# Kernel optimization log

Hardware: AMD Instinct MI355X
Metric: run time of the kernel (lower is better)

Reference implementation:

```python
import jax, jax.numpy as jnp
import numpy as np

N_NODES = 50000
N_EDGES = 600000
IN_CH = 64
HID = 128
N_GRAPHS = 64
EPS = 0.0  # GINEConv default eps


def setup_inputs() -> dict:
    key = jax.random.key(0)
    ks = jax.random.split(key, 16)
    x = jax.random.normal(ks[0], (N_NODES, IN_CH), dtype=jnp.float32)
    edge_index = jax.random.randint(ks[1], (2, N_EDGES), 0, N_NODES, dtype=jnp.int64)
    edge_attr = jax.random.normal(ks[2], (N_EDGES, 3), dtype=jnp.float32)
    batch = jnp.sort(jax.random.randint(ks[3], (N_NODES,), 0, N_GRAPHS, dtype=jnp.int64))
    s = lambda fan_in: 1.0 / np.sqrt(fan_in)
    # conv1: edge lin (3->IN_CH), mlp (IN_CH->HID->HID)
    el1_w = jax.random.uniform(ks[4], (3, IN_CH), minval=-s(3), maxval=s(3))
    el1_b = jnp.zeros((IN_CH,), jnp.float32)
    w1a = jax.random.uniform(ks[5], (IN_CH, HID), minval=-s(IN_CH), maxval=s(IN_CH))
    b1a = jnp.zeros((HID,), jnp.float32)
    w1b = jax.random.uniform(ks[6], (HID, HID), minval=-s(HID), maxval=s(HID))
    b1b = jnp.zeros((HID,), jnp.float32)
    # conv2: edge lin (3->HID), mlp (HID->HID->HID)
    el2_w = jax.random.uniform(ks[7], (3, HID), minval=-s(3), maxval=s(3))
    el2_b = jnp.zeros((HID,), jnp.float32)
    w2a = jax.random.uniform(ks[8], (HID, HID), minval=-s(HID), maxval=s(HID))
    b2a = jnp.zeros((HID,), jnp.float32)
    w2b = jax.random.uniform(ks[9], (HID, HID), minval=-s(HID), maxval=s(HID))
    b2b = jnp.zeros((HID,), jnp.float32)
    return dict(x=x, edge_index=edge_index, edge_attr=edge_attr, batch=batch,
                el1_w=el1_w, el1_b=el1_b, w1a=w1a, b1a=b1a, w1b=w1b, b1b=b1b,
                el2_w=el2_w, el2_b=el2_b, w2a=w2a, b2a=b2a, w2b=w2b, b2b=b2b)


def _gine_conv(x, src, dst, edge_attr, el_w, el_b, wa, ba, wb, bb):
    # message: relu(x_j + Lin(edge_attr)), aggregated (sum) at target nodes
    e = edge_attr @ el_w + el_b              # [E, d]
    msg = jax.nn.relu(x[src] + e)            # [E, d]
    agg = jax.ops.segment_sum(msg, dst, num_segments=x.shape[0])  # [N, d]
    h = (1.0 + EPS) * x + agg
    h = jax.nn.relu(h @ wa + ba) @ wb + bb   # MLP
    return h


def reference(x, edge_index, edge_attr, batch,
              el1_w, el1_b, w1a, b1a, w1b, b1b,
              el2_w, el2_b, w2a, b2a, w2b, b2b):
    src, dst = edge_index[0], edge_index[1]
    h = jax.nn.relu(_gine_conv(x, src, dst, edge_attr, el1_w, el1_b, w1a, b1a, w1b, b1b))
    h = jax.nn.relu(_gine_conv(h, src, dst, edge_attr, el2_w, el2_b, w2a, b2a, w2b, b2b))
    # global mean pool per graph
    sums = jax.ops.segment_sum(h, batch, num_segments=N_GRAPHS)
    cnt = jax.ops.segment_sum(jnp.ones((h.shape[0],), h.dtype), batch, num_segments=N_GRAPHS)
    return sums / jnp.maximum(cnt, 1.0)[:, None]
```

## Files before the change

kernel.cpp:

```cpp
#include <hip/hip_runtime.h>

#define N_NODES 50000
#define N_EDGES 600000
#define N_PAD 50048
#define IN_CH 64
#define HID 128
#define N_GRAPHS 64
#define CAP 64
#define CAP_SHIFT 6
#define BUILD_BLOCKS ((N_EDGES + 255) / 256)
#define PREP_BLOCKS  ((N_NODES * IN_CH / 4) / 256)

typedef __attribute__((ext_vector_type(8))) short bf16x8;
typedef __attribute__((ext_vector_type(4))) float f32x4;

__device__ __forceinline__ float bf2f(unsigned short u) {
    union { unsigned int i; float f; } v; v.i = ((unsigned int)u) << 16; return v.f;
}
__device__ __forceinline__ unsigned short f2bf(float f) {
    union { float f; unsigned int i; } v; v.f = f;
    unsigned int u = v.i;
    return (unsigned short)((u + 0x7FFFu + ((u >> 16) & 1u)) >> 16);
}


__global__ void prep_build_kernel(const float* __restrict__ x,
                                  const int* __restrict__ ei,
                                  const float* __restrict__ ea,
                                  const int* __restrict__ batch,
                                  const float* __restrict__ w1a, const float* __restrict__ w1b,
                                  const float* __restrict__ w2a, const float* __restrict__ w2b,
                                  unsigned short* __restrict__ xbf,
                                  unsigned short* __restrict__ waT1, unsigned short* __restrict__ wbT1,
                                  unsigned short* __restrict__ waT2, unsigned short* __restrict__ wbT2,
                                  int* __restrict__ deg, uint2* __restrict__ edata,
                                  float* __restrict__ out, float* __restrict__ inv_cnt) {
    const int b = blockIdx.x;
    if (b < BUILD_BLOCKS) {
        int i = b * 256 + threadIdx.x;
        if (i >= N_EDGES) return;
        int s = ei[i];
        int d = ei[N_EDGES + i];
        float a0 = ea[3 * (size_t)i], a1 = ea[3 * (size_t)i + 1], a2 = ea[3 * (size_t)i + 2];
        int p = atomicAdd(&deg[d], 1);
        if (p < CAP)
            edata[((size_t)d << CAP_SHIFT) + p] =
                make_uint2((unsigned)s | ((unsigned)f2bf(a0) << 16),
                           (unsigned)f2bf(a1) | ((unsigned)f2bf(a2) << 16));
    } else {
        int i = (b - BUILD_BLOCKS) * 256 + threadIdx.x;
        if (i < N_NODES * IN_CH / 4) {
            float4 v = ((const float4*)x)[i];
            uint2 o;
            o.x = (unsigned)f2bf(v.x) | ((unsigned)f2bf(v.y) << 16);
            o.y = (unsigned)f2bf(v.z) | ((unsigned)f2bf(v.w) << 16);
            ((uint2*)xbf)[i] = o;
        }
        if (i < N_GRAPHS * HID) out[i] = 0.f;
        if (i < N_GRAPHS) {
            int g = i;
            int lo = 0, hi = N_NODES;
            while (lo < hi) { int mid = (lo + hi) >> 1; if (batch[mid] < g) lo = mid + 1; else hi = mid; }
            int start = lo;
            lo = 0; hi = N_NODES;
            while (lo < hi) { int mid = (lo + hi) >> 1; if (batch[mid] <= g) lo = mid + 1; else hi = mid; }
            float c = (float)(lo - start);
            inv_cnt[g] = 1.0f / (c > 1.0f ? c : 1.0f);
        }
        if (i < IN_CH * HID) {
            int k = i / HID, n = i % HID;
            waT1[n * IN_CH + k] = f2bf(w1a[i]);
        }
        if (i < HID * HID) {
            int k = i / HID, n = i % HID;
            wbT1[n * HID + k] = f2bf(w1b[i]);
            waT2[n * HID + k] = f2bf(w2a[i]);
            wbT2[n * HID + k] = f2bf(w2b[i]);
        }
    }
}

__global__ __launch_bounds__(256)
void gather64_kernel(const unsigned short* __restrict__ xin,
                     const uint2* __restrict__ edata,
                     const int* __restrict__ deg,
                     const float* __restrict__ elw,
                     const float* __restrict__ elb,
                     unsigned short* __restrict__ sg) {
    const int t = threadIdx.x;
    const int w = t >> 6, l = t & 63;
    const int s = l >> 4;
    const int c = 4 * (l & 15);
    const int node = blockIdx.x * 4 + w;

    const float4 w0 = *(const float4*)&elw[c];
    const float4 w1 = *(const float4*)&elw[64 + c];
    const float4 w2 = *(const float4*)&elw[128 + c];
    const float4 eb = *(const float4*)&elb[c];

    float a0 = 0.f, a1 = 0.f, a2 = 0.f, a3 = 0.f;
    int dn = deg[node]; if (dn > CAP) dn = CAP;
    const int base = node << CAP_SHIFT;

    auto acc1 = [&](uint2 e, uint2 r, bool valid) {
        float A0 = bf2f((unsigned short)(e.x >> 16));
        float A1 = bf2f((unsigned short)(e.y & 0xFFFF));
        float A2 = bf2f((unsigned short)(e.y >> 16));
        float m0 = bf2f((unsigned short)(r.x & 0xFFFF)) + A0 * w0.x + A1 * w1.x + A2 * w2.x + eb.x;
        float m1 = bf2f((unsigned short)(r.x >> 16))    + A0 * w0.y + A1 * w1.y + A2 * w2.y + eb.y;
        float m2 = bf2f((unsigned short)(r.y & 0xFFFF)) + A0 * w0.z + A1 * w1.z + A2 * w2.z + eb.z;
        float m3 = bf2f((unsigned short)(r.y >> 16))    + A0 * w0.w + A1 * w1.w + A2 * w2.w + eb.w;
        m0 = m0 > 0.f ? m0 : 0.f;  m1 = m1 > 0.f ? m1 : 0.f;
        m2 = m2 > 0.f ? m2 : 0.f;  m3 = m3 > 0.f ? m3 : 0.f;
        a0 += valid ? m0 : 0.f;  a1 += valid ? m1 : 0.f;
        a2 += valid ? m2 : 0.f;  a3 += valid ? m3 : 0.f;
    };

    for (int j0 = 0; j0 < dn; j0 += 16) {
        uint2 e0 = edata[base + j0 + s];
        uint2 e1 = edata[base + j0 + 4 + s];
        uint2 e2 = edata[base + j0 + 8 + s];
        uint2 e3 = edata[base + j0 + 12 + s];
        bool v0 = (j0 + s) < dn,      v1 = (j0 + 4 + s) < dn;
        bool v2 = (j0 + 8 + s) < dn,  v3 = (j0 + 12 + s) < dn;
        unsigned s0 = v0 ? (e0.x & 0xFFFFu) : 0u;
        unsigned s1 = v1 ? (e1.x & 0xFFFFu) : 0u;
        unsigned s2 = v2 ? (e2.x & 0xFFFFu) : 0u;
        unsigned s3 = v3 ? (e3.x & 0xFFFFu) : 0u;
        uint2 r0 = *(const uint2*)&xin[(size_t)s0 * 64 + c];
        uint2 r1 = *(const uint2*)&xin[(size_t)s1 * 64 + c];
        uint2 r2 = *(const uint2*)&xin[(size_t)s2 * 64 + c];
        uint2 r3 = *(const uint2*)&xin[(size_t)s3 * 64 + c];
        acc1(e0, r0, v0); acc1(e1, r1, v1); acc1(e2, r2, v2); acc1(e3, r3, v3);
    }
    a0 += __shfl_xor(a0, 16); a0 += __shfl_xor(a0, 32);
    a1 += __shfl_xor(a1, 16); a1 += __shfl_xor(a1, 32);
    a2 += __shfl_xor(a2, 16); a2 += __shfl_xor(a2, 32);
    a3 += __shfl_xor(a3, 16); a3 += __shfl_xor(a3, 32);
    if (s == 0) {
        uint2 sv = *(const uint2*)&xin[(size_t)node * 64 + c];
        a0 += bf2f((unsigned short)(sv.x & 0xFFFF));
        a1 += bf2f((unsigned short)(sv.x >> 16));
        a2 += bf2f((unsigned short)(sv.y & 0xFFFF));
        a3 += bf2f((unsigned short)(sv.y >> 16));
        uint2 o;
        o.x = (unsigned)f2bf(a0) | ((unsigned)f2bf(a1) << 16);
        o.y = (unsigned)f2bf(a2) | ((unsigned)f2bf(a3) << 16);
        *(uint2*)&sg[(size_t)node * 64 + c] = o;
    }
}

__global__ __launch_bounds__(256)
void gather128_kernel(const unsigned short* __restrict__ xin,
                      const uint2* __restrict__ edata,
                      const int* __restrict__ deg,
                      const float* __restrict__ elw,
                      const float* __restrict__ elb,
                      unsigned short* __restrict__ sg) {
    const int t = threadIdx.x;
    const int w = t >> 6, l = t & 63;
    const int s = l >> 5;
    const int c = 4 * (l & 31);
    const int node = blockIdx.x * 4 + w;

    const float4 w0 = *(const float4*)&elw[c];
    const float4 w1 = *(const float4*)&elw[HID + c];
    const float4 w2 = *(const float4*)&elw[2 * HID + c];
    const float4 eb = *(const float4*)&elb[c];

    float a0 = 0.f, a1 = 0.f, a2 = 0.f, a3 = 0.f;
    int dn = deg[node]; if (dn > CAP) dn = CAP;
    const int base = node << CAP_SHIFT;

    auto acc1 = [&](uint2 e, uint2 r, bool valid) {
        float A0 = bf2f((unsigned short)(e.x >> 16));
        float A1 = bf2f((unsigned short)(e.y & 0xFFFF));
        float A2 = bf2f((unsigned short)(e.y >> 16));
        float m0 = bf2f((unsigned short)(r.x & 0xFFFF)) + A0 * w0.x + A1 * w1.x + A2 * w2.x + eb.x;
        float m1 = bf2f((unsigned short)(r.x >> 16))    + A0 * w0.y + A1 * w1.y + A2 * w2.y + eb.y;
        float m2 = bf2f((unsigned short)(r.y & 0xFFFF)) + A0 * w0.z + A1 * w1.z + A2 * w2.z + eb.z;
        float m3 = bf2f((unsigned short)(r.y >> 16))    + A0 * w0.w + A1 * w1.w + A2 * w2.w + eb.w;
        m0 = m0 > 0.f ? m0 : 0.f;  m1 = m1 > 0.f ? m1 : 0.f;
        m2 = m2 > 0.f ? m2 : 0.f;  m3 = m3 > 0.f ? m3 : 0.f;
        a0 += valid ? m0 : 0.f;  a1 += valid ? m1 : 0.f;
        a2 += valid ? m2 : 0.f;  a3 += valid ? m3 : 0.f;
    };

    for (int j0 = 0; j0 < dn; j0 += 8) {
        uint2 e0 = edata[base + j0 + s];
        uint2 e1 = edata[base + j0 + 2 + s];
        uint2 e2 = edata[base + j0 + 4 + s];
        uint2 e3 = edata[base + j0 + 6 + s];
        bool v0 = (j0 + s) < dn,      v1 = (j0 + 2 + s) < dn;
        bool v2 = (j0 + 4 + s) < dn,  v3 = (j0 + 6 + s) < dn;
        unsigned s0 = v0 ? (e0.x & 0xFFFFu) : 0u;
        unsigned s1 = v1 ? (e1.x & 0xFFFFu) : 0u;
        unsigned s2 = v2 ? (e2.x & 0xFFFFu) : 0u;
        unsigned s3 = v3 ? (e3.x & 0xFFFFu) : 0u;
        uint2 r0 = *(const uint2*)&xin[(size_t)s0 * 128 + c];
        uint2 r1 = *(const uint2*)&xin[(size_t)s1 * 128 + c];
        uint2 r2 = *(const uint2*)&xin[(size_t)s2 * 128 + c];
        uint2 r3 = *(const uint2*)&xin[(size_t)s3 * 128 + c];
        acc1(e0, r0, v0); acc1(e1, r1, v1); acc1(e2, r2, v2); acc1(e3, r3, v3);
    }
    a0 += __shfl_xor(a0, 32);
    a1 += __shfl_xor(a1, 32);
    a2 += __shfl_xor(a2, 32);
    a3 += __shfl_xor(a3, 32);
    if (s == 0) {
        uint2 sv = *(const uint2*)&xin[(size_t)node * 128 + c];
        a0 += bf2f((unsigned short)(sv.x & 0xFFFF));
        a1 += bf2f((unsigned short)(sv.x >> 16));
        a2 += bf2f((unsigned short)(sv.y & 0xFFFF));
        a3 += bf2f((unsigned short)(sv.y >> 16));
        uint2 o;
        o.x = (unsigned)f2bf(a0) | ((unsigned)f2bf(a1) << 16);
        o.y = (unsigned)f2bf(a2) | ((unsigned)f2bf(a3) << 16);
        *(uint2*)&sg[(size_t)node * 128 + c] = o;
    }
}

template <int K, bool POOL>
__global__ __launch_bounds__(256)
void mlp_mfma_kernel(const unsigned short* __restrict__ sg,
                     const unsigned short* __restrict__ waT,
                     const float* __restrict__ ba,
                     const unsigned short* __restrict__ wbT,
                     const float* __restrict__ bb,
                     void* __restrict__ outv,
                     const int* __restrict__ batch,
                     const float* __restrict__ inv_cnt) {
    constexpr int HSTR = 136;
    constexpr int OSTR = HID + 4;
    __shared__ __align__(16) unsigned short sHid[4][16 * HSTR];
    __shared__ __align__(16) float sOut[64 * OSTR];
    const int t = threadIdx.x;
    const int w = t >> 6, l = t & 63;
    const int i16 = l & 15, q = l >> 4;
    const int blk0 = blockIdx.x * 64;
    const int row0 = blk0 + w * 16;

    bf16x8 aA[K / 32];
    #pragma unroll
    for (int s = 0; s < K / 32; s++)
        aA[s] = *(const bf16x8*)&sg[(size_t)(row0 + i16) * K + s * 32 + q * 8];
    unsigned short* myHid = sHid[w];
    #pragma unroll
    for (int ct = 0; ct < 8; ct++) {
        int col = ct * 16 + i16;
        float bv = ba[col];
        f32x4 acc = (f32x4){bv, bv, bv, bv};
        #pragma unroll
        for (int s = 0; s < K / 32; s++) {
            bf16x8 b = *(const bf16x8*)&waT[(size_t)col * K + s * 32 + q * 8];
            acc = __builtin_amdgcn_mfma_f32_16x16x32_bf16(aA[s], b, acc, 0, 0, 0);
        }
        #pragma unroll
        for (int r = 0; r < 4; r++) {
            float v = acc[r] > 0.f ? acc[r] : 0.f;
            myHid[(q * 4 + r) * HSTR + col] = f2bf(v);
        }
    }
    __syncthreads();

    bf16x8 aB[4];
    #pragma unroll
    for (int s = 0; s < 4; s++)
        aB[s] = *(const bf16x8*)&myHid[i16 * HSTR + s * 32 + q * 8];
    #pragma unroll
    for (int ct = 0; ct < 8; ct++) {
        int col = ct * 16 + i16;
        float bv = bb[col];
        f32x4 acc = (f32x4){bv, bv, bv, bv};
        #pragma unroll
        for (int s = 0; s < 4; s++) {
            bf16x8 b = *(const bf16x8*)&wbT[(size_t)col * HID + s * 32 + q * 8];
            acc = __builtin_amdgcn_mfma_f32_16x16x32_bf16(aB[s], b, acc, 0, 0, 0);
        }
        #pragma unroll
        for (int r = 0; r < 4; r++) {
            float v = acc[r] > 0.f ? acc[r] : 0.f;
            sOut[(w * 16 + q * 4 + r) * OSTR + col] = v;
        }
    }
    __syncthreads();

    if (POOL) {
        if (t < HID) {
            float* out = (float*)outv;
            float acc = 0.f;
            int curg = batch[blk0];
            for (int row = 0; row < 64; row++) {
                int node = blk0 + row;
                if (node >= N_NODES) break;
                int g = batch[node];
                if (g != curg) {
                    atomicAdd(&out[curg * HID + t], acc * inv_cnt[curg]);
                    acc = 0.f; curg = g;
                }
                acc += sOut[row * OSTR + t];
            }
            atomicAdd(&out[curg * HID + t], acc * inv_cnt[curg]);
        }
    } else {
        unsigned short* hout = (unsigned short*)outv;
        for (int idx = t; idx < 64 * 16; idx += 256) {
            int row = idx >> 4, ch = idx & 15;
            int node = blk0 + row;
            if (node < N_NODES) {
                float4 f0 = *(const float4*)&sOut[row * OSTR + ch * 8];
                float4 f1 = *(const float4*)&sOut[row * OSTR + ch * 8 + 4];
                uint4 u;
                u.x = (unsigned)f2bf(f0.x) | ((unsigned)f2bf(f0.y) << 16);
                u.y = (unsigned)f2bf(f0.z) | ((unsigned)f2bf(f0.w) << 16);
                u.z = (unsigned)f2bf(f1.x) | ((unsigned)f2bf(f1.y) << 16);
                u.w = (unsigned)f2bf(f1.z) | ((unsigned)f2bf(f1.w) << 16);
                *(uint4*)&hout[(size_t)node * HID + ch * 8] = u;
            }
        }
    }
}

extern "C" void kernel_launch(void* const* d_in, const int* in_sizes, int n_in,
                              void* d_out, int out_size, void* d_ws, size_t ws_size,
                              hipStream_t stream) {
    const float* x    = (const float*)d_in[0];
    const int*   ei   = (const int*)d_in[1];
    const float* ea   = (const float*)d_in[2];
    const int*   batch= (const int*)d_in[3];
    const float* el1w = (const float*)d_in[4];
    const float* el1b = (const float*)d_in[5];
    const float* w1a  = (const float*)d_in[6];
    const float* b1a  = (const float*)d_in[7];
    const float* w1b  = (const float*)d_in[8];
    const float* b1b  = (const float*)d_in[9];
    const float* el2w = (const float*)d_in[10];
    const float* el2b = (const float*)d_in[11];
    const float* w2a  = (const float*)d_in[12];
    const float* b2a  = (const float*)d_in[13];
    const float* w2b  = (const float*)d_in[14];
    const float* b2b  = (const float*)d_in[15];
    float* out = (float*)d_out;

    uint2* edata    = (uint2*)d_ws;
    float* inv_cnt  = (float*)(edata + (size_t)N_NODES * CAP);
    int*   deg      = (int*)(inv_cnt + N_GRAPHS * HID);
    unsigned short* hbf  = (unsigned short*)((char*)inv_cnt + (size_t)58192 * 4);
    unsigned short* sgbuf= hbf + (size_t)N_NODES * HID;
    unsigned short* waT1 = sgbuf + (size_t)N_PAD * HID;
    unsigned short* wbT1 = waT1 + HID * IN_CH;
    unsigned short* waT2 = wbT1 + HID * HID;
    unsigned short* wbT2 = waT2 + HID * HID;
    unsigned short* xbf  = wbT2 + HID * HID;

    hipMemsetAsync(deg, 0, (size_t)N_NODES * sizeof(int), stream);
    prep_build_kernel<<<BUILD_BLOCKS + PREP_BLOCKS, 256, 0, stream>>>(
        x, ei, ea, batch, w1a, w1b, w2a, w2b,
        xbf, waT1, wbT1, waT2, wbT2, deg, edata, out, inv_cnt);

    gather64_kernel<<<N_NODES / 4, 256, 0, stream>>>(
        xbf, edata, deg, el1w, el1b, sgbuf);
    mlp_mfma_kernel<IN_CH, false><<<N_PAD / 64, 256, 0, stream>>>(
        sgbuf, waT1, b1a, wbT1, b1b, hbf, nullptr, nullptr);

    gather128_kernel<<<N_NODES / 4, 256, 0, stream>>>(
        hbf, edata, deg, el2w, el2b, sgbuf);
    mlp_mfma_kernel<HID, true><<<N_PAD / 64, 256, 0, stream>>>(
        sgbuf, waT2, b2a, wbT2, b2b, out, batch, inv_cnt);
}
```

Baseline: 260.1 us.

## Split gather kernels across channel slices to process more edges in parallel

The per-node gather kernels now assign each wave a 32-channel slice of a node, with 8 lanes per slice and 8 edge groups. Each loop iteration therefore covers 32 edges instead of 8 or 16, and the grid grows by 2x or 4x. This shortens the serial per-node edge loop and adds memory-level parallelism. In exchange, edge metadata is read once per slice, the reductions need an extra shuffle stage, and many lanes sit idle on low-degree nodes.

```diff
diff --git a/kernel.cpp b/kernel.cpp
--- a/kernel.cpp
+++ b/kernel.cpp
@@ -89,9 +89,10 @@
                      unsigned short* __restrict__ sg) {
     const int t = threadIdx.x;
     const int w = t >> 6, l = t & 63;
-    const int s = l >> 4;
-    const int c = 4 * (l & 15);
-    const int node = blockIdx.x * 4 + w;
+    const int s = l >> 3;
+    const int slice = blockIdx.x & 1;
+    const int c = slice * 32 + 4 * (l & 7);
+    const int node = (blockIdx.x >> 1) * 4 + w;
 
     const float4 w0 = *(const float4*)&elw[c];
     const float4 w1 = *(const float4*)&elw[64 + c];
@@ -116,13 +117,13 @@
         a2 += valid ? m2 : 0.f;  a3 += valid ? m3 : 0.f;
     };
 
-    for (int j0 = 0; j0 < dn; j0 += 16) {
+    for (int j0 = 0; j0 < dn; j0 += 32) {
         uint2 e0 = edata[base + j0 + s];
-        uint2 e1 = edata[base + j0 + 4 + s];
-        uint2 e2 = edata[base + j0 + 8 + s];
-        uint2 e3 = edata[base + j0 + 12 + s];
-        bool v0 = (j0 + s) < dn,      v1 = (j0 + 4 + s) < dn;
-        bool v2 = (j0 + 8 + s) < dn,  v3 = (j0 + 12 + s) < dn;
+        uint2 e1 = edata[base + j0 + 8 + s];
+        uint2 e2 = edata[base + j0 + 16 + s];
+        uint2 e3 = edata[base + j0 + 24 + s];
+        bool v0 = (j0 + s) < dn,       v1 = (j0 + 8 + s) < dn;
+        bool v2 = (j0 + 16 + s) < dn,  v3 = (j0 + 24 + s) < dn;
         unsigned s0 = v0 ? (e0.x & 0xFFFFu) : 0u;
         unsigned s1 = v1 ? (e1.x & 0xFFFFu) : 0u;
         unsigned s2 = v2 ? (e2.x & 0xFFFFu) : 0u;
@@ -133,10 +134,10 @@
         uint2 r3 = *(const uint2*)&xin[(size_t)s3 * 64 + c];
         acc1(e0, r0, v0); acc1(e1, r1, v1); acc1(e2, r2, v2); acc1(e3, r3, v3);
     }
-    a0 += __shfl_xor(a0, 16); a0 += __shfl_xor(a0, 32);
-    a1 += __shfl_xor(a1, 16); a1 += __shfl_xor(a1, 32);
-    a2 += __shfl_xor(a2, 16); a2 += __shfl_xor(a2, 32);
-    a3 += __shfl_xor(a3, 16); a3 += __shfl_xor(a3, 32);
+    a0 += __shfl_xor(a0, 8); a0 += __shfl_xor(a0, 16); a0 += __shfl_xor(a0, 32);
+    a1 += __shfl_xor(a1, 8); a1 += __shfl_xor(a1, 16); a1 += __shfl_xor(a1, 32);
+    a2 += __shfl_xor(a2, 8); a2 += __shfl_xor(a2, 16); a2 += __shfl_xor(a2, 32);
+    a3 += __shfl_xor(a3, 8); a3 += __shfl_xor(a3, 16); a3 += __shfl_xor(a3, 32);
     if (s == 0) {
         uint2 sv = *(const uint2*)&xin[(size_t)node * 64 + c];
         a0 += bf2f((unsigned short)(sv.x & 0xFFFF));
@@ -159,9 +160,10 @@
                       unsigned short* __restrict__ sg) {
     const int t = threadIdx.x;
     const int w = t >> 6, l = t & 63;
-    const int s = l >> 5;
-    const int c = 4 * (l & 31);
-    const int node = blockIdx.x * 4 + w;
+    const int s = l >> 3;
+    const int slice = blockIdx.x & 3;
+    const int c = slice * 32 + 4 * (l & 7);
+    const int node = (blockIdx.x >> 2) * 4 + w;
 
     const float4 w0 = *(const float4*)&elw[c];
     const float4 w1 = *(const float4*)&elw[HID + c];
@@ -186,13 +188,13 @@
         a2 += valid ? m2 : 0.f;  a3 += valid ? m3 : 0.f;
     };
 
-    for (int j0 = 0; j0 < dn; j0 += 8) {
+    for (int j0 = 0; j0 < dn; j0 += 32) {
         uint2 e0 = edata[base + j0 + s];
-        uint2 e1 = edata[base + j0 + 2 + s];
-        uint2 e2 = edata[base + j0 + 4 + s];
-        uint2 e3 = edata[base + j0 + 6 + s];
-        bool v0 = (j0 + s) < dn,      v1 = (j0 + 2 + s) < dn;
-        bool v2 = (j0 + 4 + s) < dn,  v3 = (j0 + 6 + s) < dn;
+        uint2 e1 = edata[base + j0 + 8 + s];
+        uint2 e2 = edata[base + j0 + 16 + s];
+        uint2 e3 = edata[base + j0 + 24 + s];
+        bool v0 = (j0 + s) < dn,       v1 = (j0 + 8 + s) < dn;
+        bool v2 = (j0 + 16 + s) < dn,  v3 = (j0 + 24 + s) < dn;
         unsigned s0 = v0 ? (e0.x & 0xFFFFu) : 0u;
         unsigned s1 = v1 ? (e1.x & 0xFFFFu) : 0u;
         unsigned s2 = v2 ? (e2.x & 0xFFFFu) : 0u;
@@ -203,10 +205,10 @@
         uint2 r3 = *(const uint2*)&xin[(size_t)s3 * 128 + c];
         acc1(e0, r0, v0); acc1(e1, r1, v1); acc1(e2, r2, v2); acc1(e3, r3, v3);
     }
-    a0 += __shfl_xor(a0, 32);
-    a1 += __shfl_xor(a1, 32);
-    a2 += __shfl_xor(a2, 32);
-    a3 += __shfl_xor(a3, 32);
+    a0 += __shfl_xor(a0, 8); a0 += __shfl_xor(a0, 16); a0 += __shfl_xor(a0, 32);
+    a1 += __shfl_xor(a1, 8); a1 += __shfl_xor(a1, 16); a1 += __shfl_xor(a1, 32);
+    a2 += __shfl_xor(a2, 8); a2 += __shfl_xor(a2, 16); a2 += __shfl_xor(a2, 32);
+    a3 += __shfl_xor(a3, 8); a3 += __shfl_xor(a3, 16); a3 += __shfl_xor(a3, 32);
     if (s == 0) {
         uint2 sv = *(const uint2*)&xin[(size_t)node * 128 + c];
         a0 += bf2f((unsigned short)(sv.x & 0xFFFF));
@@ -358,12 +360,12 @@
         x, ei, ea, batch, w1a, w1b, w2a, w2b,
         xbf, waT1, wbT1, waT2, wbT2, deg, edata, out, inv_cnt);
 
-    gather64_kernel<<<N_NODES / 4, 256, 0, stream>>>(
+    gather64_kernel<<<(N_NODES / 4) * 2, 256, 0, stream>>>(
         xbf, edata, deg, el1w, el1b, sgbuf);
     mlp_mfma_kernel<IN_CH, false><<<N_PAD / 64, 256, 0, stream>>>(
         sgbuf, waT1, b1a, wbT1, b1b, hbf, nullptr, nullptr);
 
-    gather128_kernel<<<N_NODES / 4, 256, 0, stream>>>(
+    gather128_kernel<<<(N_NODES / 4) * 4, 256, 0, stream>>>(
         hbf, edata, deg, el2w, el2b, sgbuf);
     mlp_mfma_kernel<HID, true><<<N_PAD / 64, 256, 0, stream>>>(
         sgbuf, waT2, b2a, wbT2, b2b, out, batch, inv_cnt);
```

Result: slower. 325.2 us (+25.0%).
